# Optimization experiments

Measured on AMD Instinct MI355X. Metric: run time of the kernel, lower is better.

The kernel has to match this reference:

```python
import jax, jax.numpy as jnp
import numpy as np

B, L, C, H, W = 8, 8, 64, 56, 56
K = 3
EPS = 1e-5


def setup_inputs() -> dict:
    key = jax.random.key(0)
    ks = jax.random.split(key, 7)
    s = lambda k, shape, sc=0.05: jax.random.normal(k, shape, dtype=jnp.float32) * sc
    return {
        "x": jax.random.normal(ks[0], (B, L, C, H, W), dtype=jnp.float32),
        "temporal_w": s(ks[1], (C, C)),        # Conv3d 1x1x1 C->C
        "temporal_b": s(ks[2], (C,)),
        "fc_w": s(ks[3], (C,)),                # Conv3d 1x1x1 C->1
        "fc_b": s(ks[4], (1,)),
        "conv_w": s(ks[5], (C, C, K, K), 0.1), # self.weight [1,1,Co,Ci,k,k] core
        "conv_b": s(ks[6], (C,)),              # self.bias [1,1,Co] core
        "bn_gamma": jnp.ones((C,), jnp.float32),
        "bn_beta": jnp.zeros((C,), jnp.float32),
    }


def reference(x, temporal_w, temporal_b, fc_w, fc_b, conv_w, conv_b, bn_gamma, bn_beta):
    b, l, c, h, w = x.shape
    # ---- generateweight_fourier ----
    xin = jnp.transpose(x, (0, 2, 1, 3, 4))                # [B,C,L,H,W]
    f = jnp.fft.fft2(xin, axes=(3, 4), norm='ortho')       # spatial FFT
    f = jnp.fft.fft(f, axis=2, norm='ortho')               # temporal FFT
    allxin = xin + 0.01 * jnp.abs(f) * xin                 # Fourier2 attention + residual
    pooled = allxin.mean(axis=(3, 4))                      # AdaptiveAvgPool3d((None,1,1)) -> [B,C,L]
    # temporalconv: 1x1x1 Conv3d C->C on [B,C,L,1,1]
    calib = jnp.einsum('oc,bcl->bol', temporal_w, pooled) + temporal_b[None, :, None]  # [B,C,L]
    # fc: 1x1x1 Conv3d C->1
    fcout = jnp.einsum('c,bcl->bl', fc_w, pooled) + fc_b[0]                            # [B,L]
    # finalweight: weight[1,1,Co,Ci,k,k] * (calib+1) broadcast over Ci -> [B,L,Co,Ci,k,k]
    calib_blc = jnp.transpose(calib, (0, 2, 1)) + 1.0      # [B,L,Ci]
    fw = conv_w[None, None] * calib_blc[:, :, None, :, None, None]
    fb = conv_b[None, None, :] * (fcout + 1.0)[:, :, None] # [B,L,Co]
    # ---- dynamic per-(sample,frame) conv2d (groups = b*l) ----
    x_flat = x.reshape(b * l, c, h, w)
    fw_flat = fw.reshape(b * l, c, c, K, K)
    fb_flat = fb.reshape(b * l, c)

    def per_sample(xi, wi):
        return jax.lax.conv_general_dilated(
            xi[None], wi, window_strides=(1, 1), padding=[(1, 1), (1, 1)],
            dimension_numbers=('NCHW', 'OIHW', 'NCHW'))[0]

    out = jax.vmap(per_sample)(x_flat, fw_flat) + fb_flat[:, :, None, None]
    out = x_flat + out                                     # residual (gate=False)
    # BatchNorm2d (training-mode batch statistics)
    mean = out.mean(axis=(0, 2, 3), keepdims=True)
    var = out.var(axis=(0, 2, 3), keepdims=True)
    out = (out - mean) * jax.lax.rsqrt(var + EPS)
    out = out * bn_gamma[None, :, None, None] + bn_beta[None, :, None, None]
    out = out * jax.nn.sigmoid(out)                        # SiLU
    return out.reshape(b, l, c, h, w)
```

## Files before the change

kernel.cpp:

```cpp
#include <hip/hip_runtime.h>
#include <cmath>

#define BB 8
#define LL 8
#define CC 64
#define HW 3136
#define NF 64
#define NBLK2 448

typedef __attribute__((ext_vector_type(8))) short short8;
typedef __attribute__((ext_vector_type(4))) float float4a;

__device__ __forceinline__ unsigned short f2bf(float f) {
    unsigned int u = __float_as_uint(f);
    u += 0x7fffu + ((u >> 16) & 1u);
    return (unsigned short)(u >> 16);
}

__global__ __launch_bounds__(256)
void pack_f_kernel(unsigned short* __restrict__ Ffix) {
    int idx = blockIdx.x * 256 + threadIdx.x;
    if (idx >= 16384) return;
    int j    = idx & 7;
    int lane = (idx >> 3) & 63;
    int ks   = (idx >> 9) & 3;
    int t    = (idx >> 11) & 3;
    int p    = (idx >> 13) & 1;
    int mn = t * 16 + (lane & 15);
    int k  = ks * 32 + (lane >> 4) * 8 + j;
    float val = 0.f;
    if (mn < 56 && k < 112) {
        int kk = (k < 56) ? k : k - 56;
        int prod = (mn * kk) % 56;
        float ang = -6.2831853071795864f * (float)prod / 56.0f;
        float cr = cosf(ang);
        float ci = sinf(ang);
        float first  = (p == 0) ? cr : ci;
        float second = (p == 0) ? -ci : cr;
        val = (k < 56) ? first : second;
    }
    Ffix[idx] = f2bf(val);
}

__global__ __launch_bounds__(256, 2)
void fft_mfma_kernel(const float* __restrict__ x,
                     const unsigned short* __restrict__ Ffix,
                     float* __restrict__ pooled) {
    const int bid = blockIdx.x;
    const int lpi = bid % 5;
    const int bc  = bid / 5;
    const int c   = bc & 63;
    const int b   = bc >> 6;
    const int lp  = lpi;
    const int tid  = threadIdx.x;
    const int lane = tid & 63;
    const int wv   = tid >> 6;
    const int n    = lane & 15;
    const int q    = lane >> 4;

    __shared__ unsigned short Tbuf[64 * 136];
    __shared__ unsigned short Ubuf[64 * 136];
    __shared__ float red[4][4];

    for (int t = tid; t < 4352; t += 256) {
        ((float*)Tbuf)[t] = 0.f;
        ((float*)Ubuf)[t] = 0.f;
    }
    __syncthreads();

    float tr[8], ti[8];
    #pragma unroll
    for (int l = 0; l < 8; ++l) {
        float ang = -6.2831853071795864f * (float)((l * lp) & 7) / 8.0f;
        tr[l] = cosf(ang);
        ti[l] = sinf(ang);
    }
    const float* xb = x + ((size_t)b * LL * CC + c) * HW;
    for (int s = tid; s < 784; s += 256) {
        int h = s / 14, w4 = s - h * 14;
        float re0 = 0.f, re1 = 0.f, re2 = 0.f, re3 = 0.f;
        float im0 = 0.f, im1 = 0.f, im2 = 0.f, im3 = 0.f;
        #pragma unroll
        for (int l = 0; l < 8; ++l) {
            float4 v = *(const float4*)(xb + (size_t)l * CC * HW + h * 56 + w4 * 4);
            re0 += v.x * tr[l]; im0 += v.x * ti[l];
            re1 += v.y * tr[l]; im1 += v.y * ti[l];
            re2 += v.z * tr[l]; im2 += v.z * ti[l];
            re3 += v.w * tr[l]; im3 += v.w * ti[l];
        }
        int w = w4 * 4;
        Tbuf[(w + 0) * 136 + h] = f2bf(re0); Tbuf[(w + 0) * 136 + 56 + h] = f2bf(im0);
        Tbuf[(w + 1) * 136 + h] = f2bf(re1); Tbuf[(w + 1) * 136 + 56 + h] = f2bf(im1);
        Tbuf[(w + 2) * 136 + h] = f2bf(re2); Tbuf[(w + 2) * 136 + 56 + h] = f2bf(im2);
        Tbuf[(w + 3) * 136 + h] = f2bf(re3); Tbuf[(w + 3) * 136 + 56 + h] = f2bf(im3);
    }
    __syncthreads();

    {
        const int p  = wv >> 1;
        const int mh = (wv & 1) * 2;
        float4a s1[2][4];
        #pragma unroll
        for (int mi = 0; mi < 2; ++mi)
            #pragma unroll
            for (int nt = 0; nt < 4; ++nt) s1[mi][nt] = (float4a){0.f, 0.f, 0.f, 0.f};
        #pragma unroll
        for (int ks = 0; ks < 4; ++ks) {
            short8 bfr[4];
            #pragma unroll
            for (int nt = 0; nt < 4; ++nt)
                bfr[nt] = *(const short8*)&Tbuf[(nt * 16 + n) * 136 + ks * 32 + q * 8];
            #pragma unroll
            for (int mi = 0; mi < 2; ++mi) {
                short8 afr = *(const short8*)(Ffix + ((((p * 4 + mh + mi) * 4 + ks) * 64 + lane) * 8));
                #pragma unroll
                for (int nt = 0; nt < 4; ++nt)
                    s1[mi][nt] = __builtin_amdgcn_mfma_f32_16x16x32_bf16(afr, bfr[nt], s1[mi][nt], 0, 0, 0);
            }
        }
        #pragma unroll
        for (int mi = 0; mi < 2; ++mi)
            #pragma unroll
            for (int nt = 0; nt < 4; ++nt)
                #pragma unroll
                for (int r = 0; r < 4; ++r) {
                    int kh = (mh + mi) * 16 + q * 4 + r;
                    int w  = nt * 16 + n;
                    if (w < 56)
                        Ubuf[kh * 136 + p * 56 + w] = f2bf(s1[mi][nt][r]);
                }
    }
    __syncthreads();

    const int mt = wv;
    short8 afr2[4];
    #pragma unroll
    for (int ks = 0; ks < 4; ++ks)
        afr2[ks] = *(const short8*)&Ubuf[(mt * 16 + n) * 136 + ks * 32 + q * 8];

    float4a g[2][4];
    #pragma unroll
    for (int pp = 0; pp < 2; ++pp)
        #pragma unroll
        for (int nt = 0; nt < 4; ++nt) g[pp][nt] = (float4a){0.f, 0.f, 0.f, 0.f};
    #pragma unroll
    for (int pp = 0; pp < 2; ++pp)
        #pragma unroll
        for (int ks = 0; ks < 4; ++ks)
            #pragma unroll
            for (int nt = 0; nt < 4; ++nt) {
                short8 bfr = *(const short8*)(Ffix + ((((pp * 4 + nt) * 4 + ks) * 64 + lane) * 8));
                g[pp][nt] = __builtin_amdgcn_mfma_f32_16x16x32_bf16(afr2[ks], bfr, g[pp][nt], 0, 0, 0);
            }

    const bool doflip = (lpi >= 1 && lpi <= 3);
    const float* x1 = x + ((size_t)((b * 8 + lp) * 64) + c) * HW;
    const float* x2 = x + ((size_t)((b * 8 + ((8 - lp) & 7)) * 64) + c) * HW;
    float S1 = 0.f, X1 = 0.f, S2 = 0.f, X2 = 0.f;
    #pragma unroll
    for (int nt = 0; nt < 4; ++nt) {
        int kw = nt * 16 + n;
        if (kw < 56) {
            int kwf = (56 - kw) % 56;
            #pragma unroll
            for (int r = 0; r < 4; ++r) {
                int kh = mt * 16 + q * 4 + r;
                if (kh < 56) {
                    float gr = g[0][nt][r], gi = g[1][nt][r];
                    float mag = sqrtf(gr * gr + gi * gi);
                    float v1 = x1[kh * 56 + kw];
                    S1 += mag * v1; X1 += v1;
                    if (doflip) {
                        int khf = (56 - kh) % 56;
                        float v2 = x2[khf * 56 + kwf];
                        S2 += mag * v2; X2 += v2;
                    }
                }
            }
        }
    }
    #pragma unroll
    for (int m = 1; m < 64; m <<= 1) {
        S1 += __shfl_xor(S1, m);
        X1 += __shfl_xor(X1, m);
        S2 += __shfl_xor(S2, m);
        X2 += __shfl_xor(X2, m);
    }
    if (lane == 0) { red[wv][0] = S1; red[wv][1] = X1; red[wv][2] = S2; red[wv][3] = X2; }
    __syncthreads();
    if (tid == 0) {
        float s1 = 0.f, xs1 = 0.f, s2 = 0.f, xs2 = 0.f;
        #pragma unroll
        for (int w = 0; w < 4; ++w) {
            s1 += red[w][0]; xs1 += red[w][1]; s2 += red[w][2]; xs2 += red[w][3];
        }
        const float kS = 0.01f / (56.0f * 2.8284271247461903f);
        pooled[bc * 8 + lp] = (xs1 + kS * s1) / 3136.0f;
        if (doflip)
            pooled[bc * 8 + (8 - lp)] = (xs2 + kS * s2) / 3136.0f;
    }
}

__global__ __launch_bounds__(64)
void calib_kernel(const float* __restrict__ pooled,
                  const float* __restrict__ tw_, const float* __restrict__ tb,
                  const float* __restrict__ fcw, const float* __restrict__ fcb,
                  const float* __restrict__ convb,
                  float* __restrict__ scale, float* __restrict__ fbias) {
    const int nn = blockIdx.x;
    const int b = nn >> 3, l = nn & 7;
    const int o = threadIdx.x;
    const float* pr = pooled + b * 512 + l;
    float dot = 0.f;
    #pragma unroll 8
    for (int c0 = 0; c0 < 64; ++c0) dot += tw_[o * 64 + c0] * pr[c0 * 8];
    float fcp = fcw[o] * pr[o * 8];
    #pragma unroll
    for (int off = 32; off > 0; off >>= 1) fcp += __shfl_down(fcp, off);
    float fcout = __shfl(fcp, 0) + fcb[0];
    scale[nn * 64 + o] = 1.0f + tb[o] + dot;
    fbias[nn * 64 + o] = convb[o] * (fcout + 1.0f);
}

__global__ __launch_bounds__(256)
void repack_w_kernel(const float* __restrict__ cw, unsigned short* __restrict__ Wp) {
    int idx = blockIdx.x * 256 + threadIdx.x;
    if (idx >= 36864) return;
    int i  = idx & 63;
    int o  = (idx >> 6) & 63;
    int kk = idx >> 12;
    Wp[idx] = f2bf(cw[(o * 64 + i) * 9 + kk]);
}

__global__ __launch_bounds__(256, 2)
void conv_mfma_kernel(const float* __restrict__ x,
                      const unsigned short* __restrict__ Wp,
                      const float* __restrict__ scale, const float* __restrict__ fbias,
                      float* __restrict__ out,
                      float* __restrict__ psum, float* __restrict__ psum2) {
    const int rt = blockIdx.x;
    const int n  = blockIdx.y;
    const int tid  = threadIdx.x;
    const int lane = tid & 63;
    const int wv   = tid >> 6;
    const int r0   = rt * 8;

    __shared__ unsigned short xs[10 * 60 * 64];
    __shared__ float fb[64], ssc[64], bn1[64], bn2[64];

    if (tid < 64) {
        fb[tid]  = fbias[n * 64 + tid];
        ssc[tid] = scale[n * 64 + tid];
        bn1[tid] = 0.f; bn2[tid] = 0.f;
    }
    __syncthreads();

    for (int t = tid; t < 10240; t += 256) {
        if (t < 8960) {
            int c4 = t % 14;
            int rr = (t / 14) % 10;
            int i  = t / 140;
            int gr = r0 - 1 + rr;
            float4 v = make_float4(0.f, 0.f, 0.f, 0.f);
            if (gr >= 0 && gr < 56)
                v = *(const float4*)(x + ((size_t)(n * 64 + i) * HW + gr * 56 + c4 * 4));
            float s = ssc[i];
            int g = i >> 3, il = i & 7;
            float vv[4] = {v.x, v.y, v.z, v.w};
            #pragma unroll
            for (int j = 0; j < 4; ++j) {
                int lc = c4 * 4 + 1 + j;
                xs[(rr * 60 + lc) * 64 + (((g ^ (lc & 7)) << 3) | il)] = f2bf(vv[j] * s);
            }
        } else {
            int idx = t - 8960;
            int i   = idx / 20;
            int rem = idx - i * 20;
            int rr  = rem >> 1;
            int lc  = (rem & 1) * 57;
            int g = i >> 3, il = i & 7;
            xs[(rr * 60 + lc) * 64 + (((g ^ (lc & 7)) << 3) | il)] = 0;
        }
    }
    __syncthreads();

    const int pxo = lane & 15;
    const int q   = lane >> 4;

    float4a acc[7][4];
    #pragma unroll
    for (int j = 0; j < 7; ++j)
        #pragma unroll
        for (int ot = 0; ot < 4; ++ot) acc[j][ot] = (float4a){0.f, 0.f, 0.f, 0.f};

    int rp[7], cp[7];
    #pragma unroll
    for (int j = 0; j < 7; ++j) {
        int px = (wv * 7 + j) * 16 + pxo;
        rp[j] = px / 56;
        cp[j] = px - rp[j] * 56;
    }

    #pragma unroll 1
    for (int kk = 0; kk < 9; ++kk) {
        const int dr = kk / 3, dc = kk - dr * 3;
        short8 a[4][2];
        #pragma unroll
        for (int ot = 0; ot < 4; ++ot)
            #pragma unroll
            for (int ih = 0; ih < 2; ++ih)
                a[ot][ih] = *(const short8*)(Wp + ((kk * 64 + ot * 16 + pxo) * 64 + ih * 32 + q * 8));

        #pragma unroll
        for (int j = 0; j < 7; ++j) {
            int lc = cp[j] + dc;
            int base = ((rp[j] + dr) * 60 + lc) * 64;
            int sw = lc & 7;
            #pragma unroll
            for (int ih = 0; ih < 2; ++ih) {
                short8 bv = *(const short8*)&xs[base + (((q + ih * 4) ^ sw) << 3)];
                #pragma unroll
                for (int ot = 0; ot < 4; ++ot)
                    acc[j][ot] = __builtin_amdgcn_mfma_f32_16x16x32_bf16(a[ot][ih], bv, acc[j][ot], 0, 0, 0);
            }
        }
    }

    float bs[4][4], bs2[4][4];
    #pragma unroll
    for (int ot = 0; ot < 4; ++ot)
        #pragma unroll
        for (int r = 0; r < 4; ++r) { bs[ot][r] = 0.f; bs2[ot][r] = 0.f; }

    #pragma unroll
    for (int j = 0; j < 7; ++j) {
        int px  = (wv * 7 + j) * 16 + pxo;
        int gpx = r0 * 56 + px;
        #pragma unroll
        for (int ot = 0; ot < 4; ++ot) {
            #pragma unroll
            for (int r = 0; r < 4; ++r) {
                int o = ot * 16 + q * 4 + r;
                size_t off = (size_t)(n * 64 + o) * HW + gpx;
                float v = acc[j][ot][r] + x[off] + fb[o];
                out[off] = v;
                bs[ot][r]  += v;
                bs2[ot][r] += v * v;
            }
        }
    }
    #pragma unroll
    for (int ot = 0; ot < 4; ++ot)
        #pragma unroll
        for (int r = 0; r < 4; ++r) {
            #pragma unroll
            for (int m = 1; m < 16; m <<= 1) {
                bs[ot][r]  += __shfl_xor(bs[ot][r], m);
                bs2[ot][r] += __shfl_xor(bs2[ot][r], m);
            }
        }
    if (pxo == 0) {
        #pragma unroll
        for (int ot = 0; ot < 4; ++ot)
            #pragma unroll
            for (int r = 0; r < 4; ++r) {
                int o = ot * 16 + q * 4 + r;
                atomicAdd(&bn1[o], bs[ot][r]);
                atomicAdd(&bn2[o], bs2[ot][r]);
            }
    }
    __syncthreads();
    if (tid < 64) {
        int bl = n * 7 + rt;
        psum[bl * 64 + tid]  = bn1[tid];
        psum2[bl * 64 + tid] = bn2[tid];
    }
}

__global__ __launch_bounds__(256)
void bnstat_kernel(const float* __restrict__ psum, const float* __restrict__ psum2,
                   float* __restrict__ bn) {
    const int o = blockIdx.x;
    const int tid = threadIdx.x;
    float s = 0.f, s2 = 0.f;
    for (int bl = tid; bl < NBLK2; bl += 256) {
        s  += psum[bl * 64 + o];
        s2 += psum2[bl * 64 + o];
    }
    __shared__ float r1[256], r2[256];
    r1[tid] = s; r2[tid] = s2;
    __syncthreads();
    for (int st = 128; st > 0; st >>= 1) {
        if (tid < st) { r1[tid] += r1[tid + st]; r2[tid] += r2[tid + st]; }
        __syncthreads();
    }
    if (tid == 0) {
        const float N = 64.0f * (float)HW;
        float mean = r1[0] / N;
        float var  = r2[0] / N - mean * mean;
        bn[o]      = mean;
        bn[64 + o] = rsqrtf(var + 1e-5f);
    }
}

__global__ __launch_bounds__(256)
void bnsilu_kernel(float* __restrict__ out, const float* __restrict__ bn,
                   const float* __restrict__ gamma, const float* __restrict__ beta) {
    size_t idx = (size_t)blockIdx.x * 256 + threadIdx.x;
    if (idx >= (size_t)NF * CC * HW) return;
    int c = (int)((idx / HW) & 63);
    float v = out[idx];
    float y = (v - bn[c]) * bn[64 + c] * gamma[c] + beta[c];
    out[idx] = y / (1.0f + expf(-y));
}

extern "C" void kernel_launch(void* const* d_in, const int* in_sizes, int n_in,
                              void* d_out, int out_size, void* d_ws, size_t ws_size,
                              hipStream_t stream) {
    const float* x          = (const float*)d_in[0];
    const float* temporal_w = (const float*)d_in[1];
    const float* temporal_b = (const float*)d_in[2];
    const float* fc_w       = (const float*)d_in[3];
    const float* fc_b       = (const float*)d_in[4];
    const float* conv_w     = (const float*)d_in[5];
    const float* conv_b     = (const float*)d_in[6];
    const float* bn_gamma   = (const float*)d_in[7];
    const float* bn_beta    = (const float*)d_in[8];
    float* out = (float*)d_out;
    float* ws  = (float*)d_ws;

    float* pooled = ws;
    float* scale  = ws + 4096;
    float* fbias  = ws + 8192;
    unsigned short* Wp = (unsigned short*)(ws + 12288);
    float* psum   = ws + 12288 + 18432;
    float* psum2  = psum + NBLK2 * 64;
    float* bn     = psum2 + NBLK2 * 64;
    unsigned short* Ffix = (unsigned short*)(bn + 128);

    pack_f_kernel<<<64, 256, 0, stream>>>(Ffix);
    repack_w_kernel<<<144, 256, 0, stream>>>(conv_w, Wp);
    fft_mfma_kernel<<<2560, 256, 0, stream>>>(x, Ffix, pooled);
    calib_kernel<<<64, 64, 0, stream>>>(pooled, temporal_w, temporal_b,
                                        fc_w, fc_b, conv_b, scale, fbias);
    conv_mfma_kernel<<<dim3(7, 64), 256, 0, stream>>>(x, Wp, scale, fbias,
                                                      out, psum, psum2);
    bnstat_kernel<<<64, 256, 0, stream>>>(psum, psum2, bn);
    int total = NF * CC * HW;
    bnsilu_kernel<<<(total + 255) / 256, 256, 0, stream>>>(out, bn, bn_gamma, bn_beta);
}
```

Measured before the change: 249.9 us.

## Stage x once per channel in LDS as bf16 and loop temporal frequencies in-block

The FFT kernel now launches one block per (batch, channel) that loads all 8 frames into shared memory as bf16 once, then loops over the 5 temporal frequencies internally. Before, 5 separate blocks each re-read the same 8 frames from global memory. The conv kernel takes its residual from the bf16 shared tile by undoing the scale, instead of re-reading x from global, and the two pack kernels are merged into one launch. The costs are lower precision on the residual and pooled sums from bf16 rounding, a large shared-memory footprint per block that may limit occupancy, and less block-level parallelism in the FFT stage.

```diff
diff --git a/kernel.cpp b/kernel.cpp
--- a/kernel.cpp
+++ b/kernel.cpp
@@ -1,9 +1,6 @@
 #include <hip/hip_runtime.h>
 #include <cmath>
 
-#define BB 8
-#define LL 8
-#define CC 64
 #define HW 3136
 #define NF 64
 #define NBLK2 448
@@ -16,188 +13,215 @@
     u += 0x7fffu + ((u >> 16) & 1u);
     return (unsigned short)(u >> 16);
 }
+__device__ __forceinline__ float bf2f(unsigned short u) {
+    return __uint_as_float(((unsigned int)u) << 16);
+}
 
 __global__ __launch_bounds__(256)
-void pack_f_kernel(unsigned short* __restrict__ Ffix) {
-    int idx = blockIdx.x * 256 + threadIdx.x;
-    if (idx >= 16384) return;
-    int j    = idx & 7;
-    int lane = (idx >> 3) & 63;
-    int ks   = (idx >> 9) & 3;
-    int t    = (idx >> 11) & 3;
-    int p    = (idx >> 13) & 1;
-    int mn = t * 16 + (lane & 15);
-    int k  = ks * 32 + (lane >> 4) * 8 + j;
-    float val = 0.f;
-    if (mn < 56 && k < 112) {
-        int kk = (k < 56) ? k : k - 56;
-        int prod = (mn * kk) % 56;
-        float ang = -6.2831853071795864f * (float)prod / 56.0f;
-        float cr = cosf(ang);
-        float ci = sinf(ang);
-        float first  = (p == 0) ? cr : ci;
-        float second = (p == 0) ? -ci : cr;
-        val = (k < 56) ? first : second;
-    }
-    Ffix[idx] = f2bf(val);
+void pack_kernel(const float* __restrict__ cw,
+                 unsigned short* __restrict__ Ffix,
+                 unsigned short* __restrict__ Wp) {
+    if (blockIdx.x < 64) {
+        int idx = blockIdx.x * 256 + threadIdx.x;
+        int j    = idx & 7;
+        int lane = (idx >> 3) & 63;
+        int ks   = (idx >> 9) & 3;
+        int t    = (idx >> 11) & 3;
+        int p    = (idx >> 13) & 1;
+        int mn = t * 16 + (lane & 15);
+        int k  = ks * 32 + (lane >> 4) * 8 + j;
+        float val = 0.f;
+        if (mn < 56 && k < 112) {
+            int kk = (k < 56) ? k : k - 56;
+            int prod = (mn * kk) % 56;
+            float ang = -6.2831853071795864f * (float)prod / 56.0f;
+            float cr = cosf(ang);
+            float ci = sinf(ang);
+            float first  = (p == 0) ? cr : ci;
+            float second = (p == 0) ? -ci : cr;
+            val = (k < 56) ? first : second;
+        }
+        Ffix[idx] = f2bf(val);
+    } else {
+        int idx = (blockIdx.x - 64) * 256 + threadIdx.x;
+        if (idx < 36864) {
+            int i  = idx & 63;
+            int o  = (idx >> 6) & 63;
+            int kk = idx >> 12;
+            Wp[idx] = f2bf(cw[(o * 64 + i) * 9 + kk]);
+        }
+    }
 }
 
 __global__ __launch_bounds__(256, 2)
 void fft_mfma_kernel(const float* __restrict__ x,
                      const unsigned short* __restrict__ Ffix,
                      float* __restrict__ pooled) {
-    const int bid = blockIdx.x;
-    const int lpi = bid % 5;
-    const int bc  = bid / 5;
-    const int c   = bc & 63;
-    const int b   = bc >> 6;
-    const int lp  = lpi;
+    const int bc = blockIdx.x;
+    const int c  = bc & 63;
+    const int b  = bc >> 6;
     const int tid  = threadIdx.x;
     const int lane = tid & 63;
     const int wv   = tid >> 6;
     const int n    = lane & 15;
     const int q    = lane >> 4;
 
-    __shared__ unsigned short Tbuf[64 * 136];
-    __shared__ unsigned short Ubuf[64 * 136];
-    __shared__ float red[4][4];
-
-    for (int t = tid; t < 4352; t += 256) {
-        ((float*)Tbuf)[t] = 0.f;
-        ((float*)Ubuf)[t] = 0.f;
+    __shared__ unsigned short sh[40352];
+    unsigned short* xbf = sh;
+    unsigned short* Tb  = sh + 25088;
+    unsigned short* Ub  = sh + 25088 + 56 * 136;
+    float* red = (float*)(sh + 40320);
+
+    for (int t = tid; t < 7616; t += 256)
+        ((unsigned int*)(sh + 25088))[t] = 0u;
+
+    for (int t = tid; t < 6272; t += 256) {
+        int l = t / 784, r = t - l * 784;
+        float4 v = *(const float4*)(x + ((size_t)((b * 8 + l) * 64 + c)) * HW + r * 4);
+        ushort4 o;
+        o.x = f2bf(v.x); o.y = f2bf(v.y); o.z = f2bf(v.z); o.w = f2bf(v.w);
+        *(ushort4*)(xbf + l * 3136 + r * 4) = o;
     }
     __syncthreads();
 
-    float tr[8], ti[8];
-    #pragma unroll
-    for (int l = 0; l < 8; ++l) {
-        float ang = -6.2831853071795864f * (float)((l * lp) & 7) / 8.0f;
-        tr[l] = cosf(ang);
-        ti[l] = sinf(ang);
-    }
-    const float* xb = x + ((size_t)b * LL * CC + c) * HW;
-    for (int s = tid; s < 784; s += 256) {
-        int h = s / 14, w4 = s - h * 14;
-        float re0 = 0.f, re1 = 0.f, re2 = 0.f, re3 = 0.f;
-        float im0 = 0.f, im1 = 0.f, im2 = 0.f, im3 = 0.f;
+    #pragma unroll 1
+    for (int lp = 0; lp < 5; ++lp) {
+        float tr[8], ti[8];
         #pragma unroll
         for (int l = 0; l < 8; ++l) {
-            float4 v = *(const float4*)(xb + (size_t)l * CC * HW + h * 56 + w4 * 4);
-            re0 += v.x * tr[l]; im0 += v.x * ti[l];
-            re1 += v.y * tr[l]; im1 += v.y * ti[l];
-            re2 += v.z * tr[l]; im2 += v.z * ti[l];
-            re3 += v.w * tr[l]; im3 += v.w * ti[l];
-        }
-        int w = w4 * 4;
-        Tbuf[(w + 0) * 136 + h] = f2bf(re0); Tbuf[(w + 0) * 136 + 56 + h] = f2bf(im0);
-        Tbuf[(w + 1) * 136 + h] = f2bf(re1); Tbuf[(w + 1) * 136 + 56 + h] = f2bf(im1);
-        Tbuf[(w + 2) * 136 + h] = f2bf(re2); Tbuf[(w + 2) * 136 + 56 + h] = f2bf(im2);
-        Tbuf[(w + 3) * 136 + h] = f2bf(re3); Tbuf[(w + 3) * 136 + 56 + h] = f2bf(im3);
-    }
-    __syncthreads();
-
-    {
-        const int p  = wv >> 1;
-        const int mh = (wv & 1) * 2;
-        float4a s1[2][4];
-        #pragma unroll
-        for (int mi = 0; mi < 2; ++mi)
-            #pragma unroll
-            for (int nt = 0; nt < 4; ++nt) s1[mi][nt] = (float4a){0.f, 0.f, 0.f, 0.f};
+            float ang = -0.78539816339744831f * (float)((l * lp) & 7);
+            tr[l] = cosf(ang);
+            ti[l] = sinf(ang);
+        }
+        for (int s = tid; s < 784; s += 256) {
+            int h = s / 14, w4 = s - h * 14;
+            float re[4] = {0.f, 0.f, 0.f, 0.f}, im[4] = {0.f, 0.f, 0.f, 0.f};
+            #pragma unroll
+            for (int l = 0; l < 8; ++l) {
+                ushort4 u = *(const ushort4*)(xbf + l * 3136 + h * 56 + w4 * 4);
+                float v0 = bf2f(u.x), v1 = bf2f(u.y), v2 = bf2f(u.z), v3 = bf2f(u.w);
+                re[0] += v0 * tr[l]; im[0] += v0 * ti[l];
+                re[1] += v1 * tr[l]; im[1] += v1 * ti[l];
+                re[2] += v2 * tr[l]; im[2] += v2 * ti[l];
+                re[3] += v3 * tr[l]; im[3] += v3 * ti[l];
+            }
+            #pragma unroll
+            for (int j = 0; j < 4; ++j) {
+                int w = w4 * 4 + j;
+                Tb[w * 136 + h]      = f2bf(re[j]);
+                Tb[w * 136 + 56 + h] = f2bf(im[j]);
+            }
+        }
+        __syncthreads();
+
+        {
+            const int p  = wv >> 1;
+            const int mh = (wv & 1) * 2;
+            float4a s1[2][4];
+            #pragma unroll
+            for (int mi = 0; mi < 2; ++mi)
+                #pragma unroll
+                for (int nt = 0; nt < 4; ++nt) s1[mi][nt] = (float4a){0.f, 0.f, 0.f, 0.f};
+            #pragma unroll
+            for (int ks = 0; ks < 4; ++ks) {
+                short8 bfr[4];
+                #pragma unroll
+                for (int nt = 0; nt < 4; ++nt) {
+                    int row = nt * 16 + n; if (row > 55) row = 55;
+                    bfr[nt] = *(const short8*)(Tb + row * 136 + ks * 32 + q * 8);
+                }
+                #pragma unroll
+                for (int mi = 0; mi < 2; ++mi) {
+                    short8 afr = *(const short8*)(Ffix + ((((p * 4 + mh + mi) * 4 + ks) * 64 + lane) * 8));
+                    #pragma unroll
+                    for (int nt = 0; nt < 4; ++nt)
+                        s1[mi][nt] = __builtin_amdgcn_mfma_f32_16x16x32_bf16(afr, bfr[nt], s1[mi][nt], 0, 0, 0);
+                }
+            }
+            #pragma unroll
+            for (int mi = 0; mi < 2; ++mi)
+                #pragma unroll
+                for (int nt = 0; nt < 4; ++nt)
+                    #pragma unroll
+                    for (int r = 0; r < 4; ++r) {
+                        int kh = (mh + mi) * 16 + q * 4 + r;
+                        int w  = nt * 16 + n;
+                        if (kh < 56 && w < 56)
+                            Ub[kh * 136 + p * 56 + w] = f2bf(s1[mi][nt][r]);
+                    }
+        }
+        __syncthreads();
+
+        const int mt = wv;
+        short8 afr2[4];
         #pragma unroll
         for (int ks = 0; ks < 4; ++ks) {
-            short8 bfr[4];
-            #pragma unroll
-            for (int nt = 0; nt < 4; ++nt)
-                bfr[nt] = *(const short8*)&Tbuf[(nt * 16 + n) * 136 + ks * 32 + q * 8];
-            #pragma unroll
-            for (int mi = 0; mi < 2; ++mi) {
-                short8 afr = *(const short8*)(Ffix + ((((p * 4 + mh + mi) * 4 + ks) * 64 + lane) * 8));
-                #pragma unroll
-                for (int nt = 0; nt < 4; ++nt)
-                    s1[mi][nt] = __builtin_amdgcn_mfma_f32_16x16x32_bf16(afr, bfr[nt], s1[mi][nt], 0, 0, 0);
-            }
-        }
-        #pragma unroll
-        for (int mi = 0; mi < 2; ++mi)
-            #pragma unroll
-            for (int nt = 0; nt < 4; ++nt)
+            int row = mt * 16 + n; if (row > 55) row = 55;
+            afr2[ks] = *(const short8*)(Ub + row * 136 + ks * 32 + q * 8);
+        }
+        float4a g[2][4];
+        #pragma unroll
+        for (int pp = 0; pp < 2; ++pp)
+            #pragma unroll
+            for (int nt = 0; nt < 4; ++nt) g[pp][nt] = (float4a){0.f, 0.f, 0.f, 0.f};
+        #pragma unroll
+        for (int pp = 0; pp < 2; ++pp)
+            #pragma unroll
+            for (int ks = 0; ks < 4; ++ks)
+                #pragma unroll
+                for (int nt = 0; nt < 4; ++nt) {
+                    short8 bfr = *(const short8*)(Ffix + ((((pp * 4 + nt) * 4 + ks) * 64 + lane) * 8));
+                    g[pp][nt] = __builtin_amdgcn_mfma_f32_16x16x32_bf16(afr2[ks], bfr, g[pp][nt], 0, 0, 0);
+                }
+
+        const bool doflip = (lp >= 1 && lp <= 3);
+        const unsigned short* x1 = xbf + lp * 3136;
+        const unsigned short* x2 = xbf + ((8 - lp) & 7) * 3136;
+        float S1 = 0.f, X1 = 0.f, S2 = 0.f, X2 = 0.f;
+        #pragma unroll
+        for (int nt = 0; nt < 4; ++nt) {
+            int kw = nt * 16 + n;
+            if (kw < 56) {
+                int kwf = (56 - kw) % 56;
                 #pragma unroll
                 for (int r = 0; r < 4; ++r) {
-                    int kh = (mh + mi) * 16 + q * 4 + r;
-                    int w  = nt * 16 + n;
-                    if (w < 56)
-                        Ubuf[kh * 136 + p * 56 + w] = f2bf(s1[mi][nt][r]);
-                }
-    }
-    __syncthreads();
-
-    const int mt = wv;
-    short8 afr2[4];
-    #pragma unroll
-    for (int ks = 0; ks < 4; ++ks)
-        afr2[ks] = *(const short8*)&Ubuf[(mt * 16 + n) * 136 + ks * 32 + q * 8];
-
-    float4a g[2][4];
-    #pragma unroll
-    for (int pp = 0; pp < 2; ++pp)
-        #pragma unroll
-        for (int nt = 0; nt < 4; ++nt) g[pp][nt] = (float4a){0.f, 0.f, 0.f, 0.f};
-    #pragma unroll
-    for (int pp = 0; pp < 2; ++pp)
-        #pragma unroll
-        for (int ks = 0; ks < 4; ++ks)
-            #pragma unroll
-            for (int nt = 0; nt < 4; ++nt) {
-                short8 bfr = *(const short8*)(Ffix + ((((pp * 4 + nt) * 4 + ks) * 64 + lane) * 8));
-                g[pp][nt] = __builtin_amdgcn_mfma_f32_16x16x32_bf16(afr2[ks], bfr, g[pp][nt], 0, 0, 0);
-            }
-
-    const bool doflip = (lpi >= 1 && lpi <= 3);
-    const float* x1 = x + ((size_t)((b * 8 + lp) * 64) + c) * HW;
-    const float* x2 = x + ((size_t)((b * 8 + ((8 - lp) & 7)) * 64) + c) * HW;
-    float S1 = 0.f, X1 = 0.f, S2 = 0.f, X2 = 0.f;
-    #pragma unroll
-    for (int nt = 0; nt < 4; ++nt) {
-        int kw = nt * 16 + n;
-        if (kw < 56) {
-            int kwf = (56 - kw) % 56;
-            #pragma unroll
-            for (int r = 0; r < 4; ++r) {
-                int kh = mt * 16 + q * 4 + r;
-                if (kh < 56) {
-                    float gr = g[0][nt][r], gi = g[1][nt][r];
-                    float mag = sqrtf(gr * gr + gi * gi);
-                    float v1 = x1[kh * 56 + kw];
-                    S1 += mag * v1; X1 += v1;
-                    if (doflip) {
-                        int khf = (56 - kh) % 56;
-                        float v2 = x2[khf * 56 + kwf];
-                        S2 += mag * v2; X2 += v2;
+                    int kh = mt * 16 + q * 4 + r;
+                    if (kh < 56) {
+                        float gr = g[0][nt][r], gi = g[1][nt][r];
+                        float mag = sqrtf(gr * gr + gi * gi);
+                        float v1 = bf2f(x1[kh * 56 + kw]);
+                        S1 += mag * v1; X1 += v1;
+                        if (doflip) {
+                            int khf = (56 - kh) % 56;
+                            float v2 = bf2f(x2[khf * 56 + kwf]);
+                            S2 += mag * v2; X2 += v2;
+                        }
                     }
                 }
             }
         }
-    }
-    #pragma unroll
-    for (int m = 1; m < 64; m <<= 1) {
-        S1 += __shfl_xor(S1, m);
-        X1 += __shfl_xor(X1, m);
-        S2 += __shfl_xor(S2, m);
-        X2 += __shfl_xor(X2, m);
-    }
-    if (lane == 0) { red[wv][0] = S1; red[wv][1] = X1; red[wv][2] = S2; red[wv][3] = X2; }
-    __syncthreads();
-    if (tid == 0) {
-        float s1 = 0.f, xs1 = 0.f, s2 = 0.f, xs2 = 0.f;
-        #pragma unroll
-        for (int w = 0; w < 4; ++w) {
-            s1 += red[w][0]; xs1 += red[w][1]; s2 += red[w][2]; xs2 += red[w][3];
-        }
-        const float kS = 0.01f / (56.0f * 2.8284271247461903f);
-        pooled[bc * 8 + lp] = (xs1 + kS * s1) / 3136.0f;
-        if (doflip)
-            pooled[bc * 8 + (8 - lp)] = (xs2 + kS * s2) / 3136.0f;
+        #pragma unroll
+        for (int m = 1; m < 64; m <<= 1) {
+            S1 += __shfl_xor(S1, m);
+            X1 += __shfl_xor(X1, m);
+            S2 += __shfl_xor(S2, m);
+            X2 += __shfl_xor(X2, m);
+        }
+        if (lane == 0) { red[wv * 4 + 0] = S1; red[wv * 4 + 1] = X1;
+                         red[wv * 4 + 2] = S2; red[wv * 4 + 3] = X2; }
+        __syncthreads();
+        if (tid == 0) {
+            float s1 = 0.f, xs1 = 0.f, s2 = 0.f, xs2 = 0.f;
+            #pragma unroll
+            for (int w = 0; w < 4; ++w) {
+                s1 += red[w * 4 + 0]; xs1 += red[w * 4 + 1];
+                s2 += red[w * 4 + 2]; xs2 += red[w * 4 + 3];
+            }
+            const float kS = 0.01f / (56.0f * 2.8284271247461903f);
+            pooled[bc * 8 + lp] = (xs1 + kS * s1) / 3136.0f;
+            if (doflip)
+                pooled[bc * 8 + (8 - lp)] = (xs2 + kS * s2) / 3136.0f;
+        }
     }
 }
 
@@ -222,16 +246,6 @@
     fbias[nn * 64 + o] = convb[o] * (fcout + 1.0f);
 }
 
-__global__ __launch_bounds__(256)
-void repack_w_kernel(const float* __restrict__ cw, unsigned short* __restrict__ Wp) {
-    int idx = blockIdx.x * 256 + threadIdx.x;
-    if (idx >= 36864) return;
-    int i  = idx & 63;
-    int o  = (idx >> 6) & 63;
-    int kk = idx >> 12;
-    Wp[idx] = f2bf(cw[(o * 64 + i) * 9 + kk]);
-}
-
 __global__ __launch_bounds__(256, 2)
 void conv_mfma_kernel(const float* __restrict__ x,
                       const unsigned short* __restrict__ Wp,
@@ -239,18 +253,20 @@
                       float* __restrict__ out,
                       float* __restrict__ psum, float* __restrict__ psum2) {
     const int rt = blockIdx.x;
-    const int n  = blockIdx.y;
+    const int nn = blockIdx.y;
     const int tid  = threadIdx.x;
     const int lane = tid & 63;
     const int wv   = tid >> 6;
     const int r0   = rt * 8;
 
     __shared__ unsigned short xs[10 * 60 * 64];
-    __shared__ float fb[64], ssc[64], bn1[64], bn2[64];
+    __shared__ float fb[64], ssc[64], rsc[64], bn1[64], bn2[64];
 
     if (tid < 64) {
-        fb[tid]  = fbias[n * 64 + tid];
-        ssc[tid] = scale[n * 64 + tid];
+        fb[tid]  = fbias[nn * 64 + tid];
+        float s  = scale[nn * 64 + tid];
+        ssc[tid] = s;
+        rsc[tid] = 1.0f / s;
         bn1[tid] = 0.f; bn2[tid] = 0.f;
     }
     __syncthreads();
@@ -263,7 +279,7 @@
             int gr = r0 - 1 + rr;
             float4 v = make_float4(0.f, 0.f, 0.f, 0.f);
             if (gr >= 0 && gr < 56)
-                v = *(const float4*)(x + ((size_t)(n * 64 + i) * HW + gr * 56 + c4 * 4));
+                v = *(const float4*)(x + ((size_t)(nn * 64 + i) * HW + gr * 56 + c4 * 4));
             float s = ssc[i];
             int g = i >> 3, il = i & 7;
             float vv[4] = {v.x, v.y, v.z, v.w};
@@ -336,13 +352,20 @@
     for (int j = 0; j < 7; ++j) {
         int px  = (wv * 7 + j) * 16 + pxo;
         int gpx = r0 * 56 + px;
+        int rr  = rp[j] + 1;
+        int lc  = cp[j] + 1;
+        int sw  = lc & 7;
+        int rowbase = (rr * 60 + lc) * 64;
         #pragma unroll
         for (int ot = 0; ot < 4; ++ot) {
+            int g  = ot * 2 + (q >> 1);
+            ushort4 uu = *(const ushort4*)(xs + rowbase + (((g ^ sw) << 3) | ((q & 1) * 4)));
+            float resid[4] = {bf2f(uu.x), bf2f(uu.y), bf2f(uu.z), bf2f(uu.w)};
             #pragma unroll
             for (int r = 0; r < 4; ++r) {
                 int o = ot * 16 + q * 4 + r;
-                size_t off = (size_t)(n * 64 + o) * HW + gpx;
-                float v = acc[j][ot][r] + x[off] + fb[o];
+                size_t off = (size_t)(nn * 64 + o) * HW + gpx;
+                float v = acc[j][ot][r] + resid[r] * rsc[o] + fb[o];
                 out[off] = v;
                 bs[ot][r]  += v;
                 bs2[ot][r] += v * v;
@@ -371,7 +394,7 @@
     }
     __syncthreads();
     if (tid < 64) {
-        int bl = n * 7 + rt;
+        int bl = nn * 7 + rt;
         psum[bl * 64 + tid]  = bn1[tid];
         psum2[bl * 64 + tid] = bn2[tid];
     }
@@ -407,7 +430,7 @@
 void bnsilu_kernel(float* __restrict__ out, const float* __restrict__ bn,
                    const float* __restrict__ gamma, const float* __restrict__ beta) {
     size_t idx = (size_t)blockIdx.x * 256 + threadIdx.x;
-    if (idx >= (size_t)NF * CC * HW) return;
+    if (idx >= (size_t)NF * 64 * HW) return;
     int c = (int)((idx / HW) & 63);
     float v = out[idx];
     float y = (v - bn[c]) * bn[64 + c] * gamma[c] + beta[c];
@@ -438,14 +461,13 @@
     float* bn     = psum2 + NBLK2 * 64;
     unsigned short* Ffix = (unsigned short*)(bn + 128);
 
-    pack_f_kernel<<<64, 256, 0, stream>>>(Ffix);
-    repack_w_kernel<<<144, 256, 0, stream>>>(conv_w, Wp);
-    fft_mfma_kernel<<<2560, 256, 0, stream>>>(x, Ffix, pooled);
+    pack_kernel<<<208, 256, 0, stream>>>(conv_w, Ffix, Wp);
+    fft_mfma_kernel<<<512, 256, 0, stream>>>(x, Ffix, pooled);
     calib_kernel<<<64, 64, 0, stream>>>(pooled, temporal_w, temporal_b,
                                         fc_w, fc_b, conv_b, scale, fbias);
     conv_mfma_kernel<<<dim3(7, 64), 256, 0, stream>>>(x, Wp, scale, fbias,
                                                       out, psum, psum2);
     bnstat_kernel<<<64, 256, 0, stream>>>(psum, psum2, bn);
-    int total = NF * CC * HW;
+    int total = NF * 64 * HW;
     bnsilu_kernel<<<(total + 255) / 256, 256, 0, stream>>>(out, bn, bn_gamma, bn_beta);
 }
```

After: 227.1 us. 1.1x faster.
